# Performance work log

Hardware: AMD Instinct MI355X
Metric: run time of the kernel (lower is better)

## Reference

```python
import jax, jax.numpy as jnp
import numpy as np

EPS = 1e-6  # matches nn.CosineSimilarity(dim=1, eps=1e-6)

def setup_inputs() -> dict:
    key = jax.random.key(0)
    k_w, k_q = jax.random.split(key)
    V, D = 1000000, 128
    weight = jax.random.normal(k_w, (V, D), dtype=jnp.float32)
    query_idx = jax.random.randint(k_q, (1,), 0, V, dtype=jnp.int64)
    return {"weight": weight, "query_idx": query_idx, "top_n": 5}

def reference(weight, query_idx, top_n):
    # weight: [V, D] embedding table; query_idx: [1] int index
    q = weight[query_idx[0]]                       # [D]
    # cosine similarity of q vs every row, torch semantics:
    # sim = x.y / clamp(||x||*||y||, min=eps)
    dots = jnp.einsum('vd,d->v', weight, q)        # [V]
    q_norm = jnp.sqrt(jnp.sum(q * q))
    w_norms = jnp.sqrt(jnp.sum(weight * weight, axis=1))  # [V]
    sim = dots / jnp.maximum(q_norm * w_norms, EPS)
    vals, idx = jax.lax.top_k(sim, top_n)          # [top_n], [top_n]
    return vals, idx
```

## Files before the change

### kernel.cpp

```cpp
#include <hip/hip_runtime.h>
#include <math.h>

#define NB1 2048
#define TPB 256
#define WAVES_PER_BLOCK (TPB / 64)
#define GROUPS_PER_WAVE 16
#define TOTAL_GROUPS (NB1 * WAVES_PER_BLOCK * GROUPS_PER_WAVE)
#define NLEAD (TPB / 4)
#define NBCAND (NLEAD * 5)
#define NCAND (NB1 * 5)

constexpr float EPS = 1e-6f;

typedef float f32x4 __attribute__((ext_vector_type(4)));

__device__ __forceinline__ bool better(float v, int i, float bv, int bi) {
    return (v > bv) || (v == bv && i < bi);
}

__device__ __forceinline__ void insert5_asc(float nv, int ni, float tv[5], int ti[5]) {
    if (nv > tv[4]) {
        #pragma unroll
        for (int j = 0; j < 5; j++) {
            bool b = better(nv, ni, tv[j], ti[j]);
            float ov = tv[j]; int oi = ti[j];
            if (b) { tv[j] = nv; ti[j] = ni; nv = ov; ni = oi; }
        }
    }
}

__device__ __forceinline__ void insert5_any(float nv, int ni, float tv[5], int ti[5]) {
    if (better(nv, ni, tv[4], ti[4])) {
        #pragma unroll
        for (int j = 0; j < 5; j++) {
            bool b = better(nv, ni, tv[j], ti[j]);
            float ov = tv[j]; int oi = ti[j];
            if (b) { tv[j] = nv; ti[j] = ni; nv = ov; ni = oi; }
        }
    }
}

__global__ __launch_bounds__(TPB) void sim_block_topk(
    const float* __restrict__ W, const int* __restrict__ qidx,
    int V, float* __restrict__ bv, int* __restrict__ bi)
{
    const int tid  = threadIdx.x;
    const int lane = tid & 63;
    const int sub  = lane & 3;
    const int grp  = lane >> 2;
    const int wave = tid >> 6;
    const int groupGlobal =
        (blockIdx.x * WAVES_PER_BLOCK + wave) * GROUPS_PER_WAVE + grp;

    const int q = qidx[0];

    f32x4 qv[8];
    const f32x4* Q4 = (const f32x4*)(W + (size_t)q * 128);
    #pragma unroll
    for (int j = 0; j < 8; j++) qv[j] = Q4[sub + 4 * j];

    float qn2 = 0.f;
    #pragma unroll
    for (int j = 0; j < 8; j++)
        qn2 += qv[j][0]*qv[j][0] + qv[j][1]*qv[j][1] + qv[j][2]*qv[j][2] + qv[j][3]*qv[j][3];
    qn2 += __shfl_xor(qn2, 1);
    qn2 += __shfl_xor(qn2, 2);
    const float qn = sqrtf(qn2);

    float tv[5]; int ti[5];
    #pragma unroll
    for (int j = 0; j < 5; j++) { tv[j] = -INFINITY; ti[j] = 0x7fffffff; }

    for (int base = groupGlobal * 2; base < V; base += 2 * TOTAL_GROUPS) {
        const f32x4* Wr = (const f32x4*)(W + (size_t)base * 128);
        f32x4 a[8], b[8];
        #pragma unroll
        for (int j = 0; j < 8; j++) a[j] = __builtin_nontemporal_load(Wr + sub + 4 * j);
        #pragma unroll
        for (int j = 0; j < 8; j++) b[j] = __builtin_nontemporal_load(Wr + 32 + sub + 4 * j);

        float dot0 = 0.f, nr0 = 0.f, dot1 = 0.f, nr1 = 0.f;
        #pragma unroll
        for (int j = 0; j < 8; j++) {
            dot0 += a[j][0]*qv[j][0] + a[j][1]*qv[j][1] + a[j][2]*qv[j][2] + a[j][3]*qv[j][3];
            nr0  += a[j][0]*a[j][0]  + a[j][1]*a[j][1]  + a[j][2]*a[j][2]  + a[j][3]*a[j][3];
        }
        #pragma unroll
        for (int j = 0; j < 8; j++) {
            dot1 += b[j][0]*qv[j][0] + b[j][1]*qv[j][1] + b[j][2]*qv[j][2] + b[j][3]*qv[j][3];
            nr1  += b[j][0]*b[j][0]  + b[j][1]*b[j][1]  + b[j][2]*b[j][2]  + b[j][3]*b[j][3];
        }
        dot0 += __shfl_xor(dot0, 1); dot0 += __shfl_xor(dot0, 2);
        nr0  += __shfl_xor(nr0,  1); nr0  += __shfl_xor(nr0,  2);
        dot1 += __shfl_xor(dot1, 1); dot1 += __shfl_xor(dot1, 2);
        nr1  += __shfl_xor(nr1,  1); nr1  += __shfl_xor(nr1,  2);

        float sim0 = dot0 / fmaxf(qn * sqrtf(nr0), EPS);
        float sim1 = dot1 / fmaxf(qn * sqrtf(nr1), EPS);
        insert5_asc(sim0, base,     tv, ti);
        insert5_asc(sim1, base + 1, tv, ti);
    }

    __shared__ float s_v[NBCAND];
    __shared__ int   s_i[NBCAND];
    __shared__ float sw_v[WAVES_PER_BLOCK];
    __shared__ int   sw_i[WAVES_PER_BLOCK], sw_p[WAVES_PER_BLOCK];

    if (sub == 0) {
        const int leader = tid >> 2;
        #pragma unroll
        for (int j = 0; j < 5; j++) { s_v[leader*5 + j] = tv[j]; s_i[leader*5 + j] = ti[j]; }
    }
    __syncthreads();

    for (int k = 0; k < 5; k++) {
        float v = -INFINITY; int i = 0x7fffffff; int p = 0;
        for (int e = tid; e < NBCAND; e += TPB) {
            if (better(s_v[e], s_i[e], v, i)) { v = s_v[e]; i = s_i[e]; p = e; }
        }
        #pragma unroll
        for (int m = 32; m >= 1; m >>= 1) {
            float ov = __shfl_xor(v, m);
            int   oi = __shfl_xor(i, m);
            int   op = __shfl_xor(p, m);
            if (better(ov, oi, v, i)) { v = ov; i = oi; p = op; }
        }
        if (lane == 0) { sw_v[wave] = v; sw_i[wave] = i; sw_p[wave] = p; }
        __syncthreads();
        if (tid == 0) {
            for (int w = 1; w < WAVES_PER_BLOCK; w++)
                if (better(sw_v[w], sw_i[w], sw_v[0], sw_i[0])) {
                    sw_v[0] = sw_v[w]; sw_i[0] = sw_i[w]; sw_p[0] = sw_p[w];
                }
            bv[blockIdx.x*5 + k] = sw_v[0];
            bi[blockIdx.x*5 + k] = sw_i[0];
            s_v[sw_p[0]] = -INFINITY;
        }
        __syncthreads();
    }
}

__global__ __launch_bounds__(256) void final_topk(
    const float* __restrict__ bv, const int* __restrict__ bi,
    float* __restrict__ out)
{
    __shared__ float s_v[TPB * 5];
    __shared__ int   s_i[TPB * 5];
    __shared__ float sw_v[4];
    __shared__ int   sw_i[4], sw_p[4];

    const int tid  = threadIdx.x;
    const int lane = tid & 63;

    float tv[5]; int ti[5];
    #pragma unroll
    for (int j = 0; j < 5; j++) { tv[j] = -INFINITY; ti[j] = 0x7fffffff; }

    for (int e = tid; e < NCAND; e += TPB)
        insert5_any(bv[e], bi[e], tv, ti);

    #pragma unroll
    for (int j = 0; j < 5; j++) { s_v[tid*5 + j] = tv[j]; s_i[tid*5 + j] = ti[j]; }
    __syncthreads();

    for (int k = 0; k < 5; k++) {
        float v = -INFINITY; int i = 0x7fffffff; int p = 0;
        for (int e = tid; e < TPB * 5; e += TPB) {
            if (better(s_v[e], s_i[e], v, i)) { v = s_v[e]; i = s_i[e]; p = e; }
        }
        #pragma unroll
        for (int m = 32; m >= 1; m >>= 1) {
            float ov = __shfl_xor(v, m);
            int   oi = __shfl_xor(i, m);
            int   op = __shfl_xor(p, m);
            if (better(ov, oi, v, i)) { v = ov; i = oi; p = op; }
        }
        if (lane == 0) { int w = tid >> 6; sw_v[w] = v; sw_i[w] = i; sw_p[w] = p; }
        __syncthreads();
        if (tid == 0) {
            for (int w = 1; w < 4; w++)
                if (better(sw_v[w], sw_i[w], sw_v[0], sw_i[0])) {
                    sw_v[0] = sw_v[w]; sw_i[0] = sw_i[w]; sw_p[0] = sw_p[w];
                }
            out[k]     = sw_v[0];
            out[5 + k] = (float)sw_i[0];
            s_v[sw_p[0]] = -INFINITY;
        }
        __syncthreads();
    }
}

extern "C" void kernel_launch(void* const* d_in, const int* in_sizes, int n_in,
                              void* d_out, int out_size, void* d_ws, size_t ws_size,
                              hipStream_t stream) {
    const float* W    = (const float*)d_in[0];
    const int*   qidx = (const int*)d_in[1];
    const int V = in_sizes[0] / 128;

    float* bv = (float*)d_ws;
    int*   bi = (int*)((char*)d_ws + (size_t)NB1 * 5 * sizeof(float));

    sim_block_topk<<<NB1, TPB, 0, stream>>>(W, qidx, V, bv, bi);
    final_topk<<<1, 256, 0, stream>>>(bv, bi, (float*)d_out);
}
```

Baseline: 670.8 us.

## Remap row work to half-wave lanes with coalesced 8-row wave chunks

Each wave now processes a contiguous chunk of 8 rows per iteration. Each half-wave of 32 lanes owns one row, and each lane reads one float4, so the loads are fully contiguous per instruction. The old layout used 4-lane groups reading strided float4s across two rows. The grid is halved to 1024 blocks, and the per-block candidate set shrinks to 8 leaders. The goal is better memory coalescing and fewer registers for the query vector. The cost is more shuffle reductions (5 levels instead of 2) and fewer concurrent rows in flight per thread.

```diff
diff --git a/kernel.cpp b/kernel.cpp
--- a/kernel.cpp
+++ b/kernel.cpp
@@ -1,13 +1,14 @@
 #include <hip/hip_runtime.h>
 #include <math.h>
 
-#define NB1 2048
+#define NB1 1024
 #define TPB 256
-#define WAVES_PER_BLOCK (TPB / 64)
-#define GROUPS_PER_WAVE 16
-#define TOTAL_GROUPS (NB1 * WAVES_PER_BLOCK * GROUPS_PER_WAVE)
-#define NLEAD (TPB / 4)
-#define NBCAND (NLEAD * 5)
+#define WPB (TPB / 64)
+#define NWAVE (NB1 * WPB)
+#define ROWS_PER_ITER 8
+#define STRIDE (NWAVE * ROWS_PER_ITER)
+#define NLEADER (WPB * 2)
+#define NBCAND (NLEADER * 5)
 #define NCAND (NB1 * 5)
 
 constexpr float EPS = 1e-6f;
@@ -44,70 +45,61 @@
     const float* __restrict__ W, const int* __restrict__ qidx,
     int V, float* __restrict__ bv, int* __restrict__ bi)
 {
-    const int tid  = threadIdx.x;
-    const int lane = tid & 63;
-    const int sub  = lane & 3;
-    const int grp  = lane >> 2;
-    const int wave = tid >> 6;
-    const int groupGlobal =
-        (blockIdx.x * WAVES_PER_BLOCK + wave) * GROUPS_PER_WAVE + grp;
+    const int tid   = threadIdx.x;
+    const int lane  = tid & 63;
+    const int wave  = tid >> 6;
+    const int hi    = lane >> 5;
+    const int hlane = lane & 31;
+    const int waveGlobal = blockIdx.x * WPB + wave;
 
     const int q = qidx[0];
 
-    f32x4 qv[8];
     const f32x4* Q4 = (const f32x4*)(W + (size_t)q * 128);
+    const f32x4 qv = Q4[hlane];
+
+    float qn2 = qv[0]*qv[0] + qv[1]*qv[1] + qv[2]*qv[2] + qv[3]*qv[3];
     #pragma unroll
-    for (int j = 0; j < 8; j++) qv[j] = Q4[sub + 4 * j];
-
-    float qn2 = 0.f;
-    #pragma unroll
-    for (int j = 0; j < 8; j++)
-        qn2 += qv[j][0]*qv[j][0] + qv[j][1]*qv[j][1] + qv[j][2]*qv[j][2] + qv[j][3]*qv[j][3];
-    qn2 += __shfl_xor(qn2, 1);
-    qn2 += __shfl_xor(qn2, 2);
+    for (int m = 1; m <= 16; m <<= 1) qn2 += __shfl_xor(qn2, m);
     const float qn = sqrtf(qn2);
 
     float tv[5]; int ti[5];
     #pragma unroll
     for (int j = 0; j < 5; j++) { tv[j] = -INFINITY; ti[j] = 0x7fffffff; }
 
-    for (int base = groupGlobal * 2; base < V; base += 2 * TOTAL_GROUPS) {
-        const f32x4* Wr = (const f32x4*)(W + (size_t)base * 128);
-        f32x4 a[8], b[8];
+    for (int chunk = waveGlobal * ROWS_PER_ITER; chunk < V; chunk += STRIDE) {
+        const f32x4* P4 = (const f32x4*)(W + (size_t)chunk * 128);
+        f32x4 a[4];
         #pragma unroll
-        for (int j = 0; j < 8; j++) a[j] = __builtin_nontemporal_load(Wr + sub + 4 * j);
+        for (int p = 0; p < 4; p++)
+            a[p] = __builtin_nontemporal_load(P4 + p * 64 + lane);
+
+        float dt[4], nr[4];
         #pragma unroll
-        for (int j = 0; j < 8; j++) b[j] = __builtin_nontemporal_load(Wr + 32 + sub + 4 * j);
-
-        float dot0 = 0.f, nr0 = 0.f, dot1 = 0.f, nr1 = 0.f;
-        #pragma unroll
-        for (int j = 0; j < 8; j++) {
-            dot0 += a[j][0]*qv[j][0] + a[j][1]*qv[j][1] + a[j][2]*qv[j][2] + a[j][3]*qv[j][3];
-            nr0  += a[j][0]*a[j][0]  + a[j][1]*a[j][1]  + a[j][2]*a[j][2]  + a[j][3]*a[j][3];
+        for (int p = 0; p < 4; p++) {
+            dt[p] = a[p][0]*qv[0] + a[p][1]*qv[1] + a[p][2]*qv[2] + a[p][3]*qv[3];
+            nr[p] = a[p][0]*a[p][0] + a[p][1]*a[p][1] + a[p][2]*a[p][2] + a[p][3]*a[p][3];
         }
         #pragma unroll
-        for (int j = 0; j < 8; j++) {
-            dot1 += b[j][0]*qv[j][0] + b[j][1]*qv[j][1] + b[j][2]*qv[j][2] + b[j][3]*qv[j][3];
-            nr1  += b[j][0]*b[j][0]  + b[j][1]*b[j][1]  + b[j][2]*b[j][2]  + b[j][3]*b[j][3];
+        for (int m = 1; m <= 16; m <<= 1) {
+            #pragma unroll
+            for (int p = 0; p < 4; p++) dt[p] += __shfl_xor(dt[p], m);
+            #pragma unroll
+            for (int p = 0; p < 4; p++) nr[p] += __shfl_xor(nr[p], m);
         }
-        dot0 += __shfl_xor(dot0, 1); dot0 += __shfl_xor(dot0, 2);
-        nr0  += __shfl_xor(nr0,  1); nr0  += __shfl_xor(nr0,  2);
-        dot1 += __shfl_xor(dot1, 1); dot1 += __shfl_xor(dot1, 2);
-        nr1  += __shfl_xor(nr1,  1); nr1  += __shfl_xor(nr1,  2);
-
-        float sim0 = dot0 / fmaxf(qn * sqrtf(nr0), EPS);
-        float sim1 = dot1 / fmaxf(qn * sqrtf(nr1), EPS);
-        insert5_asc(sim0, base,     tv, ti);
-        insert5_asc(sim1, base + 1, tv, ti);
+        #pragma unroll
+        for (int p = 0; p < 4; p++) {
+            float sim = dt[p] / fmaxf(qn * sqrtf(nr[p]), EPS);
+            insert5_asc(sim, chunk + 2 * p + hi, tv, ti);
+        }
     }
 
     __shared__ float s_v[NBCAND];
     __shared__ int   s_i[NBCAND];
-    __shared__ float sw_v[WAVES_PER_BLOCK];
-    __shared__ int   sw_i[WAVES_PER_BLOCK], sw_p[WAVES_PER_BLOCK];
+    __shared__ float sw_v[WPB];
+    __shared__ int   sw_i[WPB], sw_p[WPB];
 
-    if (sub == 0) {
-        const int leader = tid >> 2;
+    if (hlane == 0) {
+        const int leader = wave * 2 + hi;
         #pragma unroll
         for (int j = 0; j < 5; j++) { s_v[leader*5 + j] = tv[j]; s_i[leader*5 + j] = ti[j]; }
     }
@@ -128,7 +120,7 @@
         if (lane == 0) { sw_v[wave] = v; sw_i[wave] = i; sw_p[wave] = p; }
         __syncthreads();
         if (tid == 0) {
-            for (int w = 1; w < WAVES_PER_BLOCK; w++)
+            for (int w = 1; w < WPB; w++)
                 if (better(sw_v[w], sw_i[w], sw_v[0], sw_i[0])) {
                     sw_v[0] = sw_v[w]; sw_i[0] = sw_i[w]; sw_p[0] = sw_p[w];
                 }
@@ -144,8 +136,8 @@
     const float* __restrict__ bv, const int* __restrict__ bi,
     float* __restrict__ out)
 {
-    __shared__ float s_v[TPB * 5];
-    __shared__ int   s_i[TPB * 5];
+    __shared__ float s_v[256 * 5];
+    __shared__ int   s_i[256 * 5];
     __shared__ float sw_v[4];
     __shared__ int   sw_i[4], sw_p[4];
 
@@ -156,7 +148,7 @@
     #pragma unroll
     for (int j = 0; j < 5; j++) { tv[j] = -INFINITY; ti[j] = 0x7fffffff; }
 
-    for (int e = tid; e < NCAND; e += TPB)
+    for (int e = tid; e < NCAND; e += 256)
         insert5_any(bv[e], bi[e], tv, ti);
 
     #pragma unroll
@@ -165,7 +157,7 @@
 
     for (int k = 0; k < 5; k++) {
         float v = -INFINITY; int i = 0x7fffffff; int p = 0;
-        for (int e = tid; e < TPB * 5; e += TPB) {
+        for (int e = tid; e < 256 * 5; e += 256) {
             if (better(s_v[e], s_i[e], v, i)) { v = s_v[e]; i = s_i[e]; p = e; }
         }
         #pragma unroll
```

Result: faster. 641.9 us (-4.3%).
